# Kernel optimization log

Hardware: AMD Instinct MI355X
Metric: run time of the kernel (lower is better)

## Reference

```python
import jax, jax.numpy as jnp
import numpy as np


def setup_inputs() -> dict:
    key = jax.random.key(0)
    ks = jax.random.split(key, 4)
    B, T, C = 2, 4096, 512
    x = jax.random.normal(ks[0], (B, T, C), dtype=jnp.float32)
    Wqkv = jax.random.normal(ks[1], (C, 3 * C), dtype=jnp.float32) * (C ** -0.5)
    bqkv = jnp.zeros((3 * C,), dtype=jnp.float32)
    Wout = jax.random.normal(ks[2], (C, C), dtype=jnp.float32) * (C ** -0.5)
    bout = jnp.zeros((C,), dtype=jnp.float32)
    return {"x": x, "Wqkv": Wqkv, "bqkv": bqkv, "Wout": Wout, "bout": bout}


def reference(x, Wqkv, bqkv, Wout, bout):
    B, T, C = x.shape
    H = 8
    D = C // H  # head_dim
    qkv = x @ Wqkv + bqkv                       # [B, T, 3C]
    qkv = qkv.reshape(B, T, 3, H, D)
    q, k, v = qkv[:, :, 0], qkv[:, :, 1], qkv[:, :, 2]  # [B, T, H, D]
    scale = 1.0 / np.sqrt(D).astype(np.float32)
    scores = jnp.einsum("bqhd,bkhd->bhqk", q, k) * scale  # [B, H, T, T]
    causal = jnp.tril(jnp.ones((T, T), dtype=bool))
    scores = jnp.where(causal, scores, jnp.finfo(scores.dtype).min)
    attn = jax.nn.softmax(scores, axis=-1)                 # [B, H, T, T]
    out = jnp.einsum("bhqk,bkhd->bqhd", attn, v).reshape(B, T, C)
    return out @ Wout + bout
```

## Files before the change

### kernel.cpp

```cpp
#include <hip/hip_runtime.h>
#include <hip/hip_bf16.h>
#include <cstdint>
#include <cstddef>

typedef __attribute__((ext_vector_type(8))) __bf16 bf16x8;
typedef __attribute__((ext_vector_type(4))) float f32x4;
typedef __attribute__((ext_vector_type(16))) float f32x16;

__device__ __forceinline__ ushort f2b(float x) {
    union { float f; uint32_t u; } v; v.f = x;
    uint32_t r = v.u + 0x7FFFu + ((v.u >> 16) & 1u);
    return (ushort)(r >> 16);
}

__device__ __forceinline__ void glds16(const void* g, void* l) {
    __builtin_amdgcn_global_load_lds(
        (const __attribute__((address_space(1))) void*)g,
        (__attribute__((address_space(3))) void*)l, 16, 0, 0);
}

__device__ __forceinline__ uint32_t cvt_pk_bf16(float lo, float hi) {
    uint32_t r;
    asm("v_cvt_pk_bf16_f32 %0, %1, %2" : "=v"(r) : "v"(lo), "v"(hi));
    return r;
}

__device__ __forceinline__ void plane_swap(uint32_t& a, uint32_t& b) {
    asm volatile("v_permlane32_swap_b32 %0, %1" : "+v"(a), "+v"(b));
}

__device__ __forceinline__ f32x16 z16() {
    f32x16 v;
#pragma unroll
    for (int i = 0; i < 16; ++i) v[i] = 0.f;
    return v;
}

__global__ __launch_bounds__(256) void k_convert(const float* __restrict__ in,
                                                 ushort* __restrict__ out, int n8) {
    int i = blockIdx.x * 256 + threadIdx.x;
    if (i >= n8) return;
    const float4* p = (const float4*)in + (size_t)i * 2;
    float4 a = p[0], b = p[1];
    ushort o[8] = { f2b(a.x), f2b(a.y), f2b(a.z), f2b(a.w),
                    f2b(b.x), f2b(b.y), f2b(b.z), f2b(b.w) };
    *(uint4*)(out + (size_t)i * 8) = *(const uint4*)o;
}

__global__ __launch_bounds__(256) void k_transpose_w(const float* __restrict__ in,
                                                     ushort* __restrict__ out,
                                                     int R, int C) {
    __shared__ float tile[32][33];
    int c0 = blockIdx.x * 32, r0 = blockIdx.y * 32;
    int tx = threadIdx.x, ty = threadIdx.y;
#pragma unroll
    for (int i = 0; i < 32; i += 8)
        tile[ty + i][tx] = in[(size_t)(r0 + ty + i) * C + c0 + tx];
    __syncthreads();
#pragma unroll
    for (int i = 0; i < 32; i += 8)
        out[(size_t)(c0 + ty + i) * R + r0 + tx] = f2b(tile[tx][ty + i]);
}

template <int MODE>
__global__ __launch_bounds__(256) void k_gemm(const ushort* __restrict__ A,
                                              const ushort* __restrict__ BT,
                                              const float* __restrict__ bias,
                                              float* __restrict__ outF,
                                              ushort* __restrict__ Qp,
                                              ushort* __restrict__ Kp,
                                              ushort* __restrict__ VTp,
                                              int K) {
    __shared__ __align__(16) ushort lA[2][4096];
    __shared__ __align__(16) ushort lB[2][4096];
    const int tid = threadIdx.x;
    const int lane = tid & 63, lr = lane & 15, lg = lane >> 4;
    const int wid = tid >> 6, wm = wid >> 1, wn = wid & 1;
    const int m0 = blockIdx.x * 128, n0 = blockIdx.y * 128;

    const ushort* ga = A + (size_t)(m0 + (tid >> 2)) * K + (tid & 3) * 8;
    const ushort* gb = BT + (size_t)(n0 + (tid >> 2)) * K + (tid & 3) * 8;
    const size_t rstep = (size_t)64 * K;

    float bvv[4];
#pragma unroll
    for (int n = 0; n < 4; ++n) bvv[n] = bias[n0 + wn * 64 + n * 16 + lr];
    asm volatile("s_waitcnt vmcnt(0)" ::: "memory");
    __builtin_amdgcn_sched_barrier(0);

    f32x4 zero = {0.f, 0.f, 0.f, 0.f};
    f32x4 acc[4][4];
#pragma unroll
    for (int i = 0; i < 4; ++i)
#pragma unroll
        for (int j = 0; j < 4; ++j) acc[i][j] = zero;

    auto STG = [&](int buf, int k0) {
        glds16(ga + k0,         &lA[buf][tid * 8]);
        glds16(ga + k0 + rstep, &lA[buf][2048 + tid * 8]);
        glds16(gb + k0,         &lB[buf][tid * 8]);
        glds16(gb + k0 + rstep, &lB[buf][2048 + tid * 8]);
    };

    const int NT = K >> 5;
    STG(0, 0);
    for (int it = 0; it < NT; ++it) {
        const int bsel = it & 1;
        if (it + 1 < NT) {
            STG(bsel ^ 1, (it + 1) * 32);
            asm volatile("s_waitcnt vmcnt(4)" ::: "memory");
        } else {
            asm volatile("s_waitcnt vmcnt(0)" ::: "memory");
        }
        __builtin_amdgcn_sched_barrier(0);
        __builtin_amdgcn_s_barrier();
        asm volatile("" ::: "memory");

        bf16x8 af[4], bfr[4];
#pragma unroll
        for (int m = 0; m < 4; ++m)
            af[m] = *(const bf16x8*)&lA[bsel][(wm * 64 + m * 16 + lr) * 32 + lg * 8];
#pragma unroll
        for (int n = 0; n < 4; ++n)
            bfr[n] = *(const bf16x8*)&lB[bsel][(wn * 64 + n * 16 + lr) * 32 + lg * 8];
#pragma unroll
        for (int m = 0; m < 4; ++m)
#pragma unroll
            for (int n = 0; n < 4; ++n)
                acc[m][n] = __builtin_amdgcn_mfma_f32_16x16x32_bf16(af[m], bfr[n], acc[m][n], 0, 0, 0);

        asm volatile("" ::: "memory");
        __builtin_amdgcn_s_barrier();
    }

#pragma unroll
    for (int n = 0; n < 4; ++n) {
        const int gn = n0 + wn * 64 + n * 16 + lr;
        const float bv = bvv[n];
#pragma unroll
        for (int m = 0; m < 4; ++m) {
            const int gmb = m0 + wm * 64 + m * 16 + lg * 4;
            if (MODE == 0) {
                const int sec = gn >> 9, c = gn & 511;
                const int h = c >> 6, d = c & 63;
                const int b = gmb >> 12, t = gmb & 4095;
                if (sec == 2) {
                    ushort tmp[4];
#pragma unroll
                    for (int r = 0; r < 4; ++r) tmp[r] = f2b(acc[m][n][r] + bv);
                    *(ushort4*)&VTp[(size_t)(b * 8 + h) * 262144 + (size_t)d * 4096 + t] =
                        *(const ushort4*)tmp;
                } else {
                    const size_t idx0 = ((size_t)(b * 8 + h) * 4096 + t) * 64 + d;
#pragma unroll
                    for (int r = 0; r < 4; ++r) {
                        const float v = acc[m][n][r] + bv;
                        if (sec == 0) Qp[idx0 + (size_t)r * 64] = f2b(v * 0.18033688f);
                        else          Kp[idx0 + (size_t)r * 64] = f2b(v);
                    }
                }
            } else {
#pragma unroll
                for (int r = 0; r < 4; ++r)
                    outF[(size_t)(gmb + r) * 512 + gn] = acc[m][n][r] + bv;
            }
        }
    }
}

template <int MODE>
__device__ __forceinline__ void attn_run(const ushort* __restrict__ Qb,
                                         const ushort* __restrict__ Kb,
                                         const ushort* __restrict__ Vb,
                                         ushort* sm, int qt, int kv_lo, int kv_hi,
                                         int lane, int w,
                                         ushort* __restrict__ Outp, int bh,
                                         float* __restrict__ pO,
                                         float* __restrict__ pL) {
    const int lg2 = lane >> 5, l31 = lane & 31, l7 = lane & 7;
    const int q0 = qt * 128;
    const int qbase = q0 + w * 32;

    bf16x8 qf[4];
#pragma unroll
    for (int ks = 0; ks < 4; ++ks)
        qf[ks] = *(const bf16x8*)&Qb[(size_t)(qbase + l31) * 64 + ks * 16 + lg2 * 8];
    asm volatile("s_waitcnt vmcnt(0)" ::: "memory");
    __builtin_amdgcn_sched_barrier(0);

    const int srow = lane >> 3;
    const int sslot = l7 ^ srow;

    auto STAGE = [&](int buf, int kv0) {
#pragma unroll
        for (int j = 0; j < 2; ++j) {
            const int r = j * 32 + w * 8 + srow;
            glds16(Kb + (size_t)(kv0 + r) * 64 + sslot * 8,
                   (char*)sm + buf * 16384 + j * 4096 + w * 1024);
        }
#pragma unroll
        for (int j = 0; j < 2; ++j) {
            const int r = j * 32 + w * 8 + srow;
            glds16(Vb + (size_t)r * 4096 + kv0 + sslot * 8,
                   (char*)sm + buf * 16384 + 8192 + j * 4096 + w * 1024);
        }
    };

    f32x16 oacc0 = z16(), oacc1 = z16();
    float lrun = 0.f;

    STAGE(0, kv_lo * 64);
    for (int it = kv_lo; it < kv_hi; ++it) {
        const int kv0 = it * 64;
        const int bsel = (it - kv_lo) & 1;
        if (it + 1 < kv_hi) {
            STAGE(bsel ^ 1, kv0 + 64);
            asm volatile("s_waitcnt vmcnt(4)" ::: "memory");
        } else {
            asm volatile("s_waitcnt vmcnt(0)" ::: "memory");
        }
        __builtin_amdgcn_sched_barrier(0);
        __builtin_amdgcn_s_barrier();
        asm volatile("" ::: "memory");

        const bool live0 = (kv0 <= qbase + 31);
        const bool live1 = (kv0 + 32 <= qbase + 31);
        if (live0) {
            const ushort* bK = sm + bsel * 8192;
            const ushort* bV = bK + 4096;

            f32x16 st0 = z16(), st1 = z16();
            __builtin_amdgcn_s_setprio(1);
#pragma unroll
            for (int ks = 0; ks < 4; ++ks) {
                bf16x8 kf = *(const bf16x8*)&bK[l31 * 64 + (((2 * ks + lg2) ^ l7)) * 8];
                st0 = __builtin_amdgcn_mfma_f32_32x32x16_bf16(kf, qf[ks], st0, 0, 0, 0);
            }
            if (live1) {
#pragma unroll
                for (int ks = 0; ks < 4; ++ks) {
                    bf16x8 kf = *(const bf16x8*)&bK[(32 + l31) * 64 + (((2 * ks + lg2) ^ l7)) * 8];
                    st1 = __builtin_amdgcn_mfma_f32_32x32x16_bf16(kf, qf[ks], st1, 0, 0, 0);
                }
            }
            __builtin_amdgcn_s_setprio(0);
            if (kv0 == qbase) {
#pragma unroll
                for (int r = 0; r < 16; ++r) {
                    const int rowk = (r & 3) + 8 * (r >> 2) + 4 * lg2;
                    if (rowk > l31) st0[r] = -1e30f;
                }
            }
            if (live1 && kv0 + 32 == qbase) {
#pragma unroll
                for (int r = 0; r < 16; ++r) {
                    const int rowk = (r & 3) + 8 * (r >> 2) + 4 * lg2;
                    if (rowk > l31) st1[r] = -1e30f;
                }
            }

            float s0 = 0.f, s1 = 0.f, s2 = 0.f, s3 = 0.f;
#pragma unroll
            for (int r = 0; r < 16; r += 4) {
                st0[r]     = __builtin_amdgcn_exp2f(st0[r]);     s0 += st0[r];
                st0[r + 1] = __builtin_amdgcn_exp2f(st0[r + 1]); s1 += st0[r + 1];
                st0[r + 2] = __builtin_amdgcn_exp2f(st0[r + 2]); s2 += st0[r + 2];
                st0[r + 3] = __builtin_amdgcn_exp2f(st0[r + 3]); s3 += st0[r + 3];
            }
            if (live1) {
#pragma unroll
                for (int r = 0; r < 16; r += 4) {
                    st1[r]     = __builtin_amdgcn_exp2f(st1[r]);     s0 += st1[r];
                    st1[r + 1] = __builtin_amdgcn_exp2f(st1[r + 1]); s1 += st1[r + 1];
                    st1[r + 2] = __builtin_amdgcn_exp2f(st1[r + 2]); s2 += st1[r + 2];
                    st1[r + 3] = __builtin_amdgcn_exp2f(st1[r + 3]); s3 += st1[r + 3];
                }
            }
            lrun += (s0 + s1) + (s2 + s3);

#pragma unroll
            for (int stp = 0; stp < 4; ++stp) {
                if (stp >= 2 && !live1) continue;
                const int h = stp & 1;
                uint32_t a0, a1, b0, b1;
                if (stp < 2) {
                    a0 = cvt_pk_bf16(st0[h * 8 + 0], st0[h * 8 + 1]);
                    a1 = cvt_pk_bf16(st0[h * 8 + 2], st0[h * 8 + 3]);
                    b0 = cvt_pk_bf16(st0[h * 8 + 4], st0[h * 8 + 5]);
                    b1 = cvt_pk_bf16(st0[h * 8 + 6], st0[h * 8 + 7]);
                } else {
                    a0 = cvt_pk_bf16(st1[h * 8 + 0], st1[h * 8 + 1]);
                    a1 = cvt_pk_bf16(st1[h * 8 + 2], st1[h * 8 + 3]);
                    b0 = cvt_pk_bf16(st1[h * 8 + 4], st1[h * 8 + 5]);
                    b1 = cvt_pk_bf16(st1[h * 8 + 6], st1[h * 8 + 7]);
                }
                plane_swap(a0, b0);
                plane_swap(a1, b1);
                union { uint32_t u[4]; bf16x8 v; } pk;
                pk.u[0] = a0; pk.u[1] = a1; pk.u[2] = b0; pk.u[3] = b1;
                const int vs = (((2 * stp + lg2) ^ l7)) * 8;
                bf16x8 vf0 = *(const bf16x8*)&bV[l31 * 64 + vs];
                bf16x8 vf1 = *(const bf16x8*)&bV[(32 + l31) * 64 + vs];
                __builtin_amdgcn_s_setprio(1);
                oacc0 = __builtin_amdgcn_mfma_f32_32x32x16_bf16(vf0, pk.v, oacc0, 0, 0, 0);
                oacc1 = __builtin_amdgcn_mfma_f32_32x32x16_bf16(vf1, pk.v, oacc1, 0, 0, 0);
                __builtin_amdgcn_s_setprio(0);
            }
        }
        asm volatile("" ::: "memory");
        __builtin_amdgcn_s_barrier();
    }

    lrun += __shfl_xor(lrun, 32);

    if (MODE == 0) {
        const float inv = 1.0f / lrun;
        ushort* ep = sm + w * 2304;
#pragma unroll
        for (int r = 0; r < 16; ++r) {
            const int dd = (r & 3) + 8 * (r >> 2) + 4 * lg2;
            ep[l31 * 72 + dd]      = f2b(oacc0[r] * inv);
            ep[l31 * 72 + 32 + dd] = f2b(oacc1[r] * inv);
        }
        asm volatile("s_waitcnt lgkmcnt(0)" ::: "memory");
        __builtin_amdgcn_sched_barrier(0);
        const int qq = lane >> 1, half = lane & 1;
        const int bb = bh >> 3, hh = bh & 7;
        const int tg = q0 + w * 32 + qq;
        ushort* op = Outp + ((size_t)(bb * 4096 + tg) * 512 + hh * 64 + half * 32);
#pragma unroll
        for (int j = 0; j < 4; ++j) {
            uint4 v = *(const uint4*)&ep[qq * 72 + half * 32 + j * 8];
            *(uint4*)&op[j * 8] = v;
        }
    } else {
        const int qc = w * 32 + l31;
#pragma unroll
        for (int r = 0; r < 16; ++r) {
            const int dd = (r & 3) + 8 * (r >> 2) + 4 * lg2;
            pO[dd * 128 + qc]        = oacc0[r];
            pO[(dd + 32) * 128 + qc] = oacc1[r];
        }
        if (lg2 == 0) pL[qc] = lrun;
    }
}

__global__ __launch_bounds__(256) void k_attn(const ushort* __restrict__ Q,
                                              const ushort* __restrict__ K,
                                              const ushort* __restrict__ VT,
                                              ushort* __restrict__ Outp,
                                              float* __restrict__ pO,
                                              float* __restrict__ pL) {
    __shared__ __align__(16) ushort sm[16384];
    const int tid = threadIdx.x;
    const int lane = tid & 63, w = tid >> 6;
    const int bh = blockIdx.x;
    const int s = blockIdx.y;
    const int p = s >> 1, half = s & 1;
    const int qtH = 31 - p;
    const size_t base = (size_t)bh * 4096 * 64;
    const ushort* Qb = Q + base;
    const ushort* Kb = K + base;
    const ushort* Vb = VT + base;

    const size_t slot = (size_t)(bh * 16 + p) * 2 + half;
    if (half == 0) {
        attn_run<1>(Qb, Kb, Vb, sm, qtH, 0, 33, lane, w, nullptr, bh,
                    pO + slot * 8192, pL + slot * 128);
    } else {
        attn_run<1>(Qb, Kb, Vb, sm, qtH, 33, 64 - 2 * p, lane, w, nullptr, bh,
                    pO + slot * 8192, pL + slot * 128);
        attn_run<0>(Qb, Kb, Vb, sm, p, 0, 2 * p + 2, lane, w, Outp, bh,
                    nullptr, nullptr);
    }
}

__global__ __launch_bounds__(256) void k_merge(const float* __restrict__ pO,
                                               const float* __restrict__ pL,
                                               ushort* __restrict__ Outp) {
    const int bh = blockIdx.x;
    const int p = blockIdx.y;
    const int tid = threadIdx.x;
    const int q = tid >> 1, dh = (tid & 1) * 32;
    const size_t slot = (size_t)(bh * 16 + p) * 2;
    const float* OA = pO + slot * 8192;
    const float* OB = OA + 8192;
    const float la = pL[slot * 128 + q];
    const float lb = pL[slot * 128 + 128 + q];
    const float inv = 1.0f / (la + lb);
    ushort outv[32];
#pragma unroll
    for (int j = 0; j < 32; ++j) {
        const float o = (OA[(dh + j) * 128 + q] + OB[(dh + j) * 128 + q]) * inv;
        outv[j] = f2b(o);
    }
    const int b = bh >> 3, h = bh & 7;
    const int t = (31 - p) * 128 + q;
    ushort* op = Outp + ((size_t)(b * 4096 + t) * 512 + h * 64 + dh);
#pragma unroll
    for (int j = 0; j < 4; ++j) *(uint4*)&op[j * 8] = *(const uint4*)&outv[j * 8];
}

extern "C" void kernel_launch(void* const* d_in, const int* in_sizes, int n_in,
                              void* d_out, int out_size, void* d_ws, size_t ws_size,
                              hipStream_t stream) {
    const float* x    = (const float*)d_in[0];
    const float* Wqkv = (const float*)d_in[1];
    const float* bqkv = (const float*)d_in[2];
    const float* Wout = (const float*)d_in[3];
    const float* bout = (const float*)d_in[4];
    float* out = (float*)d_out;

    char* ws = (char*)d_ws;
    ushort* xb    = (ushort*)(ws);
    ushort* wqkvT = (ushort*)(ws + 8388608);
    ushort* woutT = (ushort*)(ws + 9961472);
    ushort* Qp    = (ushort*)(ws + 10485760);
    ushort* Kp    = (ushort*)(ws + 18874368);
    ushort* VTp   = (ushort*)(ws + 27262976);
    float*  pO    = (float*)(ws + 35651584);
    float*  pL    = (float*)(ws + 52428800);

    k_convert<<<2048, 256, 0, stream>>>(x, xb, 524288);
    k_transpose_w<<<dim3(48, 16), dim3(32, 8), 0, stream>>>(Wqkv, wqkvT, 512, 1536);
    k_transpose_w<<<dim3(16, 16), dim3(32, 8), 0, stream>>>(Wout, woutT, 512, 512);
    k_gemm<0><<<dim3(64, 12), 256, 0, stream>>>(xb, wqkvT, bqkv, nullptr, Qp, Kp, VTp, 512);
    k_attn<<<dim3(16, 32), 256, 0, stream>>>(Qp, Kp, VTp, xb, pO, pL);
    k_merge<<<dim3(16, 16), 256, 0, stream>>>(pO, pL, xb);
    k_gemm<1><<<dim3(64, 4), 256, 0, stream>>>(xb, woutT, bout, out, nullptr, nullptr, nullptr, 512);
}
```

Before: 109.1 us.

## Process two KV tiles per barrier pair with doubled LDS staging

```diff
diff --git a/kernel.cpp b/kernel.cpp
--- a/kernel.cpp
+++ b/kernel.cpp
@@ -191,31 +191,124 @@
     const int srow = lane >> 3;
     const int sslot = l7 ^ srow;
 
-    auto STAGE = [&](int buf, int kv0) {
+    auto STAGE = [&](int buf, int half, int kv0) {
 #pragma unroll
         for (int j = 0; j < 2; ++j) {
             const int r = j * 32 + w * 8 + srow;
             glds16(Kb + (size_t)(kv0 + r) * 64 + sslot * 8,
-                   (char*)sm + buf * 16384 + j * 4096 + w * 1024);
+                   (char*)sm + buf * 32768 + half * 16384 + j * 4096 + w * 1024);
         }
 #pragma unroll
         for (int j = 0; j < 2; ++j) {
             const int r = j * 32 + w * 8 + srow;
             glds16(Vb + (size_t)r * 4096 + kv0 + sslot * 8,
-                   (char*)sm + buf * 16384 + 8192 + j * 4096 + w * 1024);
+                   (char*)sm + buf * 32768 + half * 16384 + 8192 + j * 4096 + w * 1024);
         }
     };
 
     f32x16 oacc0 = z16(), oacc1 = z16();
     float lrun = 0.f;
 
-    STAGE(0, kv_lo * 64);
-    for (int it = kv_lo; it < kv_hi; ++it) {
+    auto UNIT = [&](int buf, int half, int it) {
         const int kv0 = it * 64;
-        const int bsel = (it - kv_lo) & 1;
-        if (it + 1 < kv_hi) {
-            STAGE(bsel ^ 1, kv0 + 64);
-            asm volatile("s_waitcnt vmcnt(4)" ::: "memory");
+        const bool live0 = (kv0 <= qbase + 31);
+        const bool live1 = (kv0 + 32 <= qbase + 31);
+        if (!live0) return;
+        const ushort* bK = sm + buf * 16384 + half * 8192;
+        const ushort* bV = bK + 4096;
+
+        f32x16 st0 = z16(), st1 = z16();
+#pragma unroll
+        for (int ks = 0; ks < 4; ++ks) {
+            bf16x8 kf = *(const bf16x8*)&bK[l31 * 64 + (((2 * ks + lg2) ^ l7)) * 8];
+            st0 = __builtin_amdgcn_mfma_f32_32x32x16_bf16(kf, qf[ks], st0, 0, 0, 0);
+        }
+        if (live1) {
+#pragma unroll
+            for (int ks = 0; ks < 4; ++ks) {
+                bf16x8 kf = *(const bf16x8*)&bK[(32 + l31) * 64 + (((2 * ks + lg2) ^ l7)) * 8];
+                st1 = __builtin_amdgcn_mfma_f32_32x32x16_bf16(kf, qf[ks], st1, 0, 0, 0);
+            }
+        }
+        if (kv0 == qbase) {
+#pragma unroll
+            for (int r = 0; r < 16; ++r) {
+                const int rowk = (r & 3) + 8 * (r >> 2) + 4 * lg2;
+                if (rowk > l31) st0[r] = -1e30f;
+            }
+        }
+        if (live1 && kv0 + 32 == qbase) {
+#pragma unroll
+            for (int r = 0; r < 16; ++r) {
+                const int rowk = (r & 3) + 8 * (r >> 2) + 4 * lg2;
+                if (rowk > l31) st1[r] = -1e30f;
+            }
+        }
+
+        float s0 = 0.f, s1 = 0.f, s2 = 0.f, s3 = 0.f;
+#pragma unroll
+        for (int r = 0; r < 16; r += 4) {
+            st0[r]     = __builtin_amdgcn_exp2f(st0[r]);     s0 += st0[r];
+            st0[r + 1] = __builtin_amdgcn_exp2f(st0[r + 1]); s1 += st0[r + 1];
+            st0[r + 2] = __builtin_amdgcn_exp2f(st0[r + 2]); s2 += st0[r + 2];
+            st0[r + 3] = __builtin_amdgcn_exp2f(st0[r + 3]); s3 += st0[r + 3];
+        }
+        if (live1) {
+#pragma unroll
+            for (int r = 0; r < 16; r += 4) {
+                st1[r]     = __builtin_amdgcn_exp2f(st1[r]);     s0 += st1[r];
+                st1[r + 1] = __builtin_amdgcn_exp2f(st1[r + 1]); s1 += st1[r + 1];
+                st1[r + 2] = __builtin_amdgcn_exp2f(st1[r + 2]); s2 += st1[r + 2];
+                st1[r + 3] = __builtin_amdgcn_exp2f(st1[r + 3]); s3 += st1[r + 3];
+            }
+        }
+        lrun += (s0 + s1) + (s2 + s3);
+
+#pragma unroll
+        for (int stp = 0; stp < 4; ++stp) {
+            if (stp >= 2 && !live1) continue;
+            const int h = stp & 1;
+            uint32_t a0, a1, b0, b1;
+            if (stp < 2) {
+                a0 = cvt_pk_bf16(st0[h * 8 + 0], st0[h * 8 + 1]);
+                a1 = cvt_pk_bf16(st0[h * 8 + 2], st0[h * 8 + 3]);
+                b0 = cvt_pk_bf16(st0[h * 8 + 4], st0[h * 8 + 5]);
+                b1 = cvt_pk_bf16(st0[h * 8 + 6], st0[h * 8 + 7]);
+            } else {
+                a0 = cvt_pk_bf16(st1[h * 8 + 0], st1[h * 8 + 1]);
+                a1 = cvt_pk_bf16(st1[h * 8 + 2], st1[h * 8 + 3]);
+                b0 = cvt_pk_bf16(st1[h * 8 + 4], st1[h * 8 + 5]);
+                b1 = cvt_pk_bf16(st1[h * 8 + 6], st1[h * 8 + 7]);
+            }
+            plane_swap(a0, b0);
+            plane_swap(a1, b1);
+            union { uint32_t u[4]; bf16x8 v; } pk;
+            pk.u[0] = a0; pk.u[1] = a1; pk.u[2] = b0; pk.u[3] = b1;
+            const int vs = (((2 * stp + lg2) ^ l7)) * 8;
+            bf16x8 vf0 = *(const bf16x8*)&bV[l31 * 64 + vs];
+            bf16x8 vf1 = *(const bf16x8*)&bV[(32 + l31) * 64 + vs];
+            oacc0 = __builtin_amdgcn_mfma_f32_32x32x16_bf16(vf0, pk.v, oacc0, 0, 0, 0);
+            oacc1 = __builtin_amdgcn_mfma_f32_32x32x16_bf16(vf1, pk.v, oacc1, 0, 0, 0);
+        }
+    };
+
+    const int n = kv_hi - kv_lo;
+    const int ng = (n + 1) >> 1;
+
+    STAGE(0, 0, kv_lo * 64);
+    if (n > 1) STAGE(0, 1, (kv_lo + 1) * 64);
+
+    for (int g = 0; g < ng; ++g) {
+        const int bsel = g & 1;
+        if (g + 1 < ng) {
+            const int u = kv_lo + 2 * (g + 1);
+            STAGE(bsel ^ 1, 0, u * 64);
+            if (2 * (g + 1) + 1 < n) {
+                STAGE(bsel ^ 1, 1, (u + 1) * 64);
+                asm volatile("s_waitcnt vmcnt(8)" ::: "memory");
+            } else {
+                asm volatile("s_waitcnt vmcnt(4)" ::: "memory");
+            }
         } else {
             asm volatile("s_waitcnt vmcnt(0)" ::: "memory");
         }
@@ -223,90 +316,9 @@
         __builtin_amdgcn_s_barrier();
         asm volatile("" ::: "memory");
 
-        const bool live0 = (kv0 <= qbase + 31);
-        const bool live1 = (kv0 + 32 <= qbase + 31);
-        if (live0) {
-            const ushort* bK = sm + bsel * 8192;
-            const ushort* bV = bK + 4096;
-
-            f32x16 st0 = z16(), st1 = z16();
-            __builtin_amdgcn_s_setprio(1);
-#pragma unroll
-            for (int ks = 0; ks < 4; ++ks) {
-                bf16x8 kf = *(const bf16x8*)&bK[l31 * 64 + (((2 * ks + lg2) ^ l7)) * 8];
-                st0 = __builtin_amdgcn_mfma_f32_32x32x16_bf16(kf, qf[ks], st0, 0, 0, 0);
-            }
-            if (live1) {
-#pragma unroll
-                for (int ks = 0; ks < 4; ++ks) {
-                    bf16x8 kf = *(const bf16x8*)&bK[(32 + l31) * 64 + (((2 * ks + lg2) ^ l7)) * 8];
-                    st1 = __builtin_amdgcn_mfma_f32_32x32x16_bf16(kf, qf[ks], st1, 0, 0, 0);
-                }
-            }
-            __builtin_amdgcn_s_setprio(0);
-            if (kv0 == qbase) {
-#pragma unroll
-                for (int r = 0; r < 16; ++r) {
-                    const int rowk = (r & 3) + 8 * (r >> 2) + 4 * lg2;
-                    if (rowk > l31) st0[r] = -1e30f;
-                }
-            }
-            if (live1 && kv0 + 32 == qbase) {
-#pragma unroll
-                for (int r = 0; r < 16; ++r) {
-                    const int rowk = (r & 3) + 8 * (r >> 2) + 4 * lg2;
-                    if (rowk > l31) st1[r] = -1e30f;
-                }
-            }
-
-            float s0 = 0.f, s1 = 0.f, s2 = 0.f, s3 = 0.f;
-#pragma unroll
-            for (int r = 0; r < 16; r += 4) {
-                st0[r]     = __builtin_amdgcn_exp2f(st0[r]);     s0 += st0[r];
-                st0[r + 1] = __builtin_amdgcn_exp2f(st0[r + 1]); s1 += st0[r + 1];
-                st0[r + 2] = __builtin_amdgcn_exp2f(st0[r + 2]); s2 += st0[r + 2];
-                st0[r + 3] = __builtin_amdgcn_exp2f(st0[r + 3]); s3 += st0[r + 3];
-            }
-            if (live1) {
-#pragma unroll
-                for (int r = 0; r < 16; r += 4) {
-                    st1[r]     = __builtin_amdgcn_exp2f(st1[r]);     s0 += st1[r];
-                    st1[r + 1] = __builtin_amdgcn_exp2f(st1[r + 1]); s1 += st1[r + 1];
-                    st1[r + 2] = __builtin_amdgcn_exp2f(st1[r + 2]); s2 += st1[r + 2];
-                    st1[r + 3] = __builtin_amdgcn_exp2f(st1[r + 3]); s3 += st1[r + 3];
-                }
-            }
-            lrun += (s0 + s1) + (s2 + s3);
-
-#pragma unroll
-            for (int stp = 0; stp < 4; ++stp) {
-                if (stp >= 2 && !live1) continue;
-                const int h = stp & 1;
-                uint32_t a0, a1, b0, b1;
-                if (stp < 2) {
-                    a0 = cvt_pk_bf16(st0[h * 8 + 0], st0[h * 8 + 1]);
-                    a1 = cvt_pk_bf16(st0[h * 8 + 2], st0[h * 8 + 3]);
-                    b0 = cvt_pk_bf16(st0[h * 8 + 4], st0[h * 8 + 5]);
-                    b1 = cvt_pk_bf16(st0[h * 8 + 6], st0[h * 8 + 7]);
-                } else {
-                    a0 = cvt_pk_bf16(st1[h * 8 + 0], st1[h * 8 + 1]);
-                    a1 = cvt_pk_bf16(st1[h * 8 + 2], st1[h * 8 + 3]);
-                    b0 = cvt_pk_bf16(st1[h * 8 + 4], st1[h * 8 + 5]);
-                    b1 = cvt_pk_bf16(st1[h * 8 + 6], st1[h * 8 + 7]);
-                }
-                plane_swap(a0, b0);
-                plane_swap(a1, b1);
-                union { uint32_t u[4]; bf16x8 v; } pk;
-                pk.u[0] = a0; pk.u[1] = a1; pk.u[2] = b0; pk.u[3] = b1;
-                const int vs = (((2 * stp + lg2) ^ l7)) * 8;
-                bf16x8 vf0 = *(const bf16x8*)&bV[l31 * 64 + vs];
-                bf16x8 vf1 = *(const bf16x8*)&bV[(32 + l31) * 64 + vs];
-                __builtin_amdgcn_s_setprio(1);
-                oacc0 = __builtin_amdgcn_mfma_f32_32x32x16_bf16(vf0, pk.v, oacc0, 0, 0, 0);
-                oacc1 = __builtin_amdgcn_mfma_f32_32x32x16_bf16(vf1, pk.v, oacc1, 0, 0, 0);
-                __builtin_amdgcn_s_setprio(0);
-            }
-        }
+        UNIT(bsel, 0, kv_lo + 2 * g);
+        if (2 * g + 1 < n) UNIT(bsel, 1, kv_lo + 2 * g + 1);
+
         asm volatile("" ::: "memory");
         __builtin_amdgcn_s_barrier();
     }
@@ -351,7 +363,7 @@
                                               ushort* __restrict__ Outp,
                                               float* __restrict__ pO,
                                               float* __restrict__ pL) {
-    __shared__ __align__(16) ushort sm[16384];
+    __shared__ __align__(16) ushort sm[32768];
     const int tid = threadIdx.x;
     const int lane = tid & 63, w = tid >> 6;
     const int bh = blockIdx.x;
```

Result: no change. 111.3 us (+2.0%).
